# Performance work log

Hardware: AMD Instinct MI355X
Metric: run time of the kernel (lower is better)

Reference implementation:

```python
import jax, jax.numpy as jnp
import numpy as np

N_NODES = 50000
N_EDGES = 800000
EPS = 1e-12


def _l2norm(x):
    # F.normalize(x, p=2, dim=1)
    n = jnp.sqrt(jnp.sum(x * x, axis=1, keepdims=True))
    return x / jnp.maximum(n, EPS)


def _sage_layer(h, src, dst, inv_deg, W_self, W_neigh, b, last):
    # mean aggregation over in-neighbors: gather src feats, scatter-add to dst
    msg = jax.ops.segment_sum(h[src], dst, num_segments=N_NODES)  # [N, d]
    h_neigh = msg * inv_deg  # [N, d]
    rst = h @ W_self + h_neigh @ W_neigh + b
    if not last:
        rst = jax.nn.relu(rst)
        rst = _l2norm(rst)
    return rst


def setup_inputs() -> dict:
    key = jax.random.key(0)
    ks = jax.random.split(key, 10)
    d_in, d_h, d_out = 128, 128, 64
    s = lambda k, sh, fan: jax.random.normal(k, sh, jnp.float32) / np.sqrt(fan)
    return {
        "features": jax.random.normal(ks[0], (N_NODES, d_in), jnp.float32),
        "src": jax.random.randint(ks[1], (N_EDGES,), 0, N_NODES, jnp.int32),
        "dst": jax.random.randint(ks[2], (N_EDGES,), 0, N_NODES, jnp.int32),
        "W_self0": s(ks[3], (d_in, d_h), d_in),
        "W_neigh0": s(ks[4], (d_in, d_h), d_in),
        "b0": jnp.zeros((d_h,), jnp.float32),
        "W_self1": s(ks[5], (d_h, d_h), d_h),
        "W_neigh1": s(ks[6], (d_h, d_h), d_h),
        "b1": jnp.zeros((d_h,), jnp.float32),
        "W_self2": s(ks[7], (d_h, d_out), d_h),
        "W_neigh2": s(ks[8], (d_h, d_out), d_h),
        "b2": jnp.zeros((d_out,), jnp.float32),
    }


def reference(features, src, dst, W_self0, W_neigh0, b0, W_self1, W_neigh1, b1, W_self2, W_neigh2, b2):
    # in-degree for mean aggregation (clamped to avoid div-by-zero)
    deg = jax.ops.segment_sum(jnp.ones((N_EDGES,), jnp.float32), dst, num_segments=N_NODES)
    inv_deg = (1.0 / jnp.maximum(deg, 1.0))[:, None]  # [N,1]
    h = _sage_layer(features, src, dst, inv_deg, W_self0, W_neigh0, b0, last=False)
    h = _sage_layer(h, src, dst, inv_deg, W_self1, W_neigh1, b1, last=False)
    out = _sage_layer(h, src, dst, inv_deg, W_self2, W_neigh2, b2, last=True)
    return out
```

## Files before the change

### kernel.cpp

```cpp
#include <hip/hip_runtime.h>
#include <hip/hip_bf16.h>

#define N_NODES 50000
#define N_EDGES 800000
#define NBUCKET 196
#define NPB 256
#define BUCKET_CAP 7168
#define BUCKET_PAD 8192
#define PART_EDGES 4096
#define PART_BLOCKS ((N_EDGES + PART_EDGES - 1) / PART_EDGES)
#define SENTINEL 0xFFFFFFFFu

typedef __attribute__((ext_vector_type(8))) short bf16x8;
typedef __attribute__((ext_vector_type(4))) float f32x4;

__device__ __forceinline__ float bf2f(unsigned short u) {
    unsigned int x = ((unsigned int)u) << 16;
    return __uint_as_float(x);
}
__device__ __forceinline__ unsigned short f2bf(float f) {
    unsigned int x = __float_as_uint(f);
    unsigned int lsb = (x >> 16) & 1u;
    x += 0x7fffu + lsb;
    return (unsigned short)(x >> 16);
}

#define NF2 ((N_NODES * 64 + 255) / 256)
__global__ __launch_bounds__(256) void k_prep(
        const float* __restrict__ Ws0, const float* __restrict__ Wn0,
        const float* __restrict__ Ws1, const float* __restrict__ Wn1,
        const float* __restrict__ Ws2, const float* __restrict__ Wn2,
        __hip_bfloat16* __restrict__ frag0, __hip_bfloat16* __restrict__ frag1,
        __hip_bfloat16* __restrict__ frag2,
        const float2* __restrict__ fin, unsigned int* __restrict__ fout,
        unsigned int* __restrict__ z1, unsigned int* __restrict__ z2,
        int* __restrict__ cursor, int* __restrict__ valid) {
    int b = blockIdx.x;
    if (b >= 40 + NF2) {
        int tid = threadIdx.x;
        if (tid < NBUCKET) { cursor[tid] = 0; valid[tid] = 0; }
        if (tid < 64)       fout[(size_t)N_NODES * 64 + tid] = 0;
        else if (tid < 128) z1[(size_t)N_NODES * 64 + (tid - 64)] = 0;
        else if (tid < 192) z2[(size_t)N_NODES * 64 + (tid - 128)] = 0;
        return;
    }
    if (b >= 40) {
        int i = (b - 40) * 256 + threadIdx.x;
        if (i < N_NODES * 64) {
            float2 v = fin[i];
            fout[i] = ((unsigned int)f2bf(v.y) << 16) | (unsigned int)f2bf(v.x);
        }
        return;
    }
    const float* Wself;
    const float* Wneigh;
    __hip_bfloat16* frag;
    int Dout, lb;
    if (b < 16)      { Wself = Ws0; Wneigh = Wn0; frag = frag0; Dout = 128; lb = b; }
    else if (b < 32) { Wself = Ws1; Wneigh = Wn1; frag = frag1; Dout = 128; lb = b - 16; }
    else             { Wself = Ws2; Wneigh = Wn2; frag = frag2; Dout = 64;  lb = b - 32; }
    int t = lb * 256 + threadIdx.x;
    int nCt = Dout >> 4;
    int total = nCt * 8 * 64;
    if (t >= total) return;
    int lane = t & 63;
    int kt = (t >> 6) & 7;
    int ct = t >> 9;
    int q = lane >> 4;
    int n = ct * 16 + (lane & 15);
    unsigned short* dstp = (unsigned short*)frag + ((size_t)((ct * 8 + kt) * 64 + lane)) * 8;
    #pragma unroll
    for (int j = 0; j < 8; ++j) {
        int k = kt * 32 + q * 8 + j;
        float v = (k < 128) ? Wself[k * Dout + n] : Wneigh[(k - 128) * Dout + n];
        dstp[j] = f2bf(v);
    }
}

__global__ __launch_bounds__(256) void k_zero(int* __restrict__ cursor, int* __restrict__ valid) {
    int tid = threadIdx.x;
    if (tid < NBUCKET) { cursor[tid] = 0; valid[tid] = 0; }
}

__global__ __launch_bounds__(256) void k_partA(const int* __restrict__ src,
                                               const int* __restrict__ dst,
                                               int* __restrict__ cursor,
                                               int* __restrict__ valid,
                                               unsigned int* __restrict__ bucketArr) {
    __shared__ int hist[NBUCKET];
    __shared__ int base[NBUCKET];
    __shared__ int cnt[NBUCKET];
    int tid = threadIdx.x;
    if (tid < NBUCKET) hist[tid] = 0;
    __syncthreads();
    int e0 = blockIdx.x * PART_EDGES;
    for (int j = 0; j < PART_EDGES; j += 256) {
        int e = e0 + j + tid;
        if (e < N_EDGES) atomicAdd(&hist[dst[e] >> 8], 1);
    }
    __syncthreads();
    if (tid < NBUCKET) {
        int h = hist[tid];
        int hp = (h + 15) & ~15;
        int b0 = atomicAdd(&cursor[tid], hp);
        atomicAdd(&valid[tid], h);
        base[tid] = b0;
        cnt[tid] = 0;
        for (int k = h; k < hp; ++k) {
            int p = b0 + k;
            if (p < BUCKET_CAP) bucketArr[(size_t)tid * BUCKET_CAP + p] = SENTINEL;
        }
    }
    __syncthreads();
    for (int j = 0; j < PART_EDGES; j += 256) {
        int e = e0 + j + tid;
        if (e < N_EDGES) {
            int d = dst[e];
            int b = d >> 8;
            int p = base[b] + atomicAdd(&cnt[b], 1);
            if (p < BUCKET_CAP)
                bucketArr[(size_t)b * BUCKET_CAP + p] =
                    (unsigned int)src[e] | ((unsigned int)(d & 255) << 16);
        }
    }
}

__global__ __launch_bounds__(256) void k_partB(const unsigned int* __restrict__ bucketArr,
                                               const int* __restrict__ cursor,
                                               int* __restrict__ off_beg,
                                               int* __restrict__ off_end,
                                               float* __restrict__ inv_deg,
                                               int* __restrict__ edge_src) {
    __shared__ unsigned int ed[BUCKET_CAP];
    __shared__ int csr[BUCKET_CAP];
    __shared__ int hist[256];
    __shared__ int lbase[256];
    __shared__ int lcnt[256];
    __shared__ int tot_s;
    int b = blockIdx.x;
    int tid = threadIdx.x;
    int size = min(cursor[b], BUCKET_CAP);
    int B0 = b * BUCKET_PAD;
    int nbase = b * NPB;
    int ncount = min(NPB, N_NODES - nbase);
    hist[tid] = 0;
    __syncthreads();
    for (int j = 0; j < BUCKET_CAP; j += 256) {
        int i = j + tid;
        if (i < size) {
            unsigned int u = bucketArr[(size_t)b * BUCKET_CAP + i];
            ed[i] = u;
            if ((u >> 16) < 256u) atomicAdd(&hist[u >> 16], 1);
        }
    }
    __syncthreads();
    int v = hist[tid];
    int pv = (v + 15) & ~15;
    lbase[tid] = pv;
    __syncthreads();
    for (int off = 1; off < 256; off <<= 1) {
        int t = (tid >= off) ? lbase[tid - off] : 0;
        __syncthreads();
        lbase[tid] += t;
        __syncthreads();
    }
    int excl = lbase[tid] - pv;
    if (tid == 255) tot_s = lbase[255];
    __syncthreads();
    lbase[tid] = excl;
    lcnt[tid] = 0;
    if (tid < ncount) {
        off_beg[nbase + tid] = B0 + excl;
        off_end[nbase + tid] = B0 + excl + pv;
        inv_deg[nbase + tid] = 1.0f / (float)max(v, 1);
    }
    __syncthreads();
    int tot = min(tot_s, BUCKET_CAP);
    for (int j = tid; j < tot; j += 256) csr[j] = N_NODES;
    __syncthreads();
    for (int j = 0; j < BUCKET_CAP; j += 256) {
        int i = j + tid;
        if (i < size) {
            unsigned int u = ed[i];
            unsigned int ld = u >> 16;
            if (ld < 256u) {
                int p = lbase[ld] + atomicAdd(&lcnt[ld], 1);
                if (p < BUCKET_CAP) csr[p] = (int)(u & 0xffffu);
            }
        }
    }
    __syncthreads();
    for (int j = tid; j < tot; j += 256) edge_src[B0 + j] = csr[j];
}

__global__ void k_agg(const __hip_bfloat16* __restrict__ hv,
                      const int* __restrict__ off_beg, const int* __restrict__ off_end,
                      const int* __restrict__ edge_src, const float* __restrict__ inv_deg,
                      __hip_bfloat16* __restrict__ msg) {
    int gid = blockIdx.x * blockDim.x + threadIdx.x;
    int node = gid >> 6;
    int lane = gid & 63;
    if (node >= N_NODES) return;
    int quad = lane >> 4;
    int sub = lane & 15;
    int beg = off_beg[node], endp = off_end[node];
    const uint4* hp = (const uint4*)hv;

    float a0[8], a1[8], a2[8], a3[8];
    #pragma unroll
    for (int c = 0; c < 8; ++c) { a0[c] = 0.f; a1[c] = 0.f; a2[c] = 0.f; a3[c] = 0.f; }

    for (int i = beg; i < endp; i += 16) {
        int s0 = edge_src[i + quad];
        int s1 = edge_src[i + 4 + quad];
        int s2 = edge_src[i + 8 + quad];
        int s3 = edge_src[i + 12 + quad];
        uint4 u0 = hp[(size_t)s0 * 16 + sub];
        uint4 u1 = hp[(size_t)s1 * 16 + sub];
        uint4 u2 = hp[(size_t)s2 * 16 + sub];
        uint4 u3 = hp[(size_t)s3 * 16 + sub];
        a0[0] += bf2f((unsigned short)(u0.x & 0xffffu)); a0[1] += bf2f((unsigned short)(u0.x >> 16));
        a0[2] += bf2f((unsigned short)(u0.y & 0xffffu)); a0[3] += bf2f((unsigned short)(u0.y >> 16));
        a0[4] += bf2f((unsigned short)(u0.z & 0xffffu)); a0[5] += bf2f((unsigned short)(u0.z >> 16));
        a0[6] += bf2f((unsigned short)(u0.w & 0xffffu)); a0[7] += bf2f((unsigned short)(u0.w >> 16));
        a1[0] += bf2f((unsigned short)(u1.x & 0xffffu)); a1[1] += bf2f((unsigned short)(u1.x >> 16));
        a1[2] += bf2f((unsigned short)(u1.y & 0xffffu)); a1[3] += bf2f((unsigned short)(u1.y >> 16));
        a1[4] += bf2f((unsigned short)(u1.z & 0xffffu)); a1[5] += bf2f((unsigned short)(u1.z >> 16));
        a1[6] += bf2f((unsigned short)(u1.w & 0xffffu)); a1[7] += bf2f((unsigned short)(u1.w >> 16));
        a2[0] += bf2f((unsigned short)(u2.x & 0xffffu)); a2[1] += bf2f((unsigned short)(u2.x >> 16));
        a2[2] += bf2f((unsigned short)(u2.y & 0xffffu)); a2[3] += bf2f((unsigned short)(u2.y >> 16));
        a2[4] += bf2f((unsigned short)(u2.z & 0xffffu)); a2[5] += bf2f((unsigned short)(u2.z >> 16));
        a2[6] += bf2f((unsigned short)(u2.w & 0xffffu)); a2[7] += bf2f((unsigned short)(u2.w >> 16));
        a3[0] += bf2f((unsigned short)(u3.x & 0xffffu)); a3[1] += bf2f((unsigned short)(u3.x >> 16));
        a3[2] += bf2f((unsigned short)(u3.y & 0xffffu)); a3[3] += bf2f((unsigned short)(u3.y >> 16));
        a3[4] += bf2f((unsigned short)(u3.z & 0xffffu)); a3[5] += bf2f((unsigned short)(u3.z >> 16));
        a3[6] += bf2f((unsigned short)(u3.w & 0xffffu)); a3[7] += bf2f((unsigned short)(u3.w >> 16));
    }

    float r[8];
    #pragma unroll
    for (int c = 0; c < 8; ++c) {
        float t = a0[c] + a1[c] + a2[c] + a3[c];
        t += __shfl_xor(t, 16);
        t += __shfl_xor(t, 32);
        r[c] = t;
    }
    if (quad == 0) {
        float w = inv_deg[node];
        uint4 o;
        o.x = ((unsigned int)f2bf(r[1] * w) << 16) | (unsigned int)f2bf(r[0] * w);
        o.y = ((unsigned int)f2bf(r[3] * w) << 16) | (unsigned int)f2bf(r[2] * w);
        o.z = ((unsigned int)f2bf(r[5] * w) << 16) | (unsigned int)f2bf(r[4] * w);
        o.w = ((unsigned int)f2bf(r[7] * w) << 16) | (unsigned int)f2bf(r[6] * w);
        ((uint4*)msg)[(size_t)node * 16 + sub] = o;
    }
}

template <int NCT, bool LAST>
__global__ __launch_bounds__(256) void k_gemm(const __hip_bfloat16* __restrict__ Aself,
                                              const __hip_bfloat16* __restrict__ Aneigh,
                                              const __hip_bfloat16* __restrict__ frag,
                                              const float* __restrict__ bias,
                                              void* __restrict__ out_) {
    constexpr int Dout = NCT * 16;
    int tid = threadIdx.x;
    int wv = tid >> 6, lane = tid & 63;
    int n0 = blockIdx.x * 64 + wv * 16;
    if (n0 >= N_NODES) return;
    int q = lane >> 4, l15 = lane & 15;
    int rowA = n0 + l15;
    if (rowA > N_NODES - 1) rowA = N_NODES - 1;

    f32x4 acc[NCT];
    #pragma unroll
    for (int c = 0; c < NCT; ++c) acc[c] = (f32x4){0.f, 0.f, 0.f, 0.f};

    const bf16x8* fragv = (const bf16x8*)frag;
    #pragma unroll
    for (int kt = 0; kt < 8; ++kt) {
        int kb = (kt & 3) * 32 + q * 8;
        const __hip_bfloat16* Ab = (kt < 4) ? Aself : Aneigh;
        bf16x8 a = *(const bf16x8*)(Ab + (size_t)rowA * 128 + kb);
        #pragma unroll
        for (int ct = 0; ct < NCT; ++ct) {
            bf16x8 b = fragv[(ct * 8 + kt) * 64 + lane];
            acc[ct] = __builtin_amdgcn_mfma_f32_16x16x32_bf16(a, b, acc[ct], 0, 0, 0);
        }
    }

    float ss[4] = {0.f, 0.f, 0.f, 0.f};
    #pragma unroll
    for (int ct = 0; ct < NCT; ++ct) {
        float bc = bias[ct * 16 + l15];
        #pragma unroll
        for (int r = 0; r < 4; ++r) {
            float v = acc[ct][r] + bc;
            if (!LAST) v = fmaxf(v, 0.0f);
            acc[ct][r] = v;
            ss[r] += v * v;
        }
    }

    float scale[4];
    #pragma unroll
    for (int r = 0; r < 4; ++r) {
        if (!LAST) {
            float s = ss[r];
            s += __shfl_xor(s, 1);
            s += __shfl_xor(s, 2);
            s += __shfl_xor(s, 4);
            s += __shfl_xor(s, 8);
            scale[r] = 1.0f / fmaxf(sqrtf(s), 1e-12f);
        } else {
            scale[r] = 1.0f;
        }
    }

    #pragma unroll
    for (int ct = 0; ct < NCT; ++ct) {
        #pragma unroll
        for (int r = 0; r < 4; ++r) {
            int row = n0 + q * 4 + r;
            if (row < N_NODES) {
                float v = acc[ct][r] * scale[r];
                if (LAST)
                    ((float*)out_)[(size_t)row * Dout + ct * 16 + l15] = v;
                else
                    ((unsigned short*)out_)[(size_t)row * Dout + ct * 16 + l15] = f2bf(v);
            }
        }
    }
}


extern "C" void kernel_launch(void* const* d_in, const int* in_sizes, int n_in,
                              void* d_out, int out_size, void* d_ws, size_t ws_size,
                              hipStream_t stream) {
    const float* features = (const float*)d_in[0];
    const int* src = (const int*)d_in[1];
    const int* dst = (const int*)d_in[2];
    const float* Ws0 = (const float*)d_in[3];
    const float* Wn0 = (const float*)d_in[4];
    const float* b0  = (const float*)d_in[5];
    const float* Ws1 = (const float*)d_in[6];
    const float* Wn1 = (const float*)d_in[7];
    const float* b1  = (const float*)d_in[8];
    const float* Ws2 = (const float*)d_in[9];
    const float* Wn2 = (const float*)d_in[10];
    const float* b2  = (const float*)d_in[11];
    float* out = (float*)d_out;

    char* ws = (char*)d_ws;
    size_t off = 0;
    auto alloc = [&](size_t bytes) -> void* {
        void* p = ws + off;
        off = (off + bytes + 255) & ~(size_t)255;
        return p;
    };
    int*   cursor   = (int*)alloc((size_t)NBUCKET * 4);
    int*   valid    = (int*)alloc((size_t)NBUCKET * 4);
    unsigned int* bucketArr = (unsigned int*)alloc((size_t)NBUCKET * BUCKET_CAP * 4);
    int*   off_beg  = (int*)alloc((size_t)N_NODES * 4);
    int*   off_end  = (int*)alloc((size_t)N_NODES * 4);
    int*   edge_src = (int*)alloc((size_t)NBUCKET * BUCKET_PAD * 4);
    float* inv_deg  = (float*)alloc((size_t)N_NODES * 4);
    __hip_bfloat16* fbf = (__hip_bfloat16*)alloc((size_t)(N_NODES + 1) * 128 * 2);
    __hip_bfloat16* msg = (__hip_bfloat16*)alloc((size_t)N_NODES * 128 * 2);
    __hip_bfloat16* h1  = (__hip_bfloat16*)alloc((size_t)(N_NODES + 1) * 128 * 2);
    __hip_bfloat16* h2  = (__hip_bfloat16*)alloc((size_t)(N_NODES + 1) * 128 * 2);
    __hip_bfloat16* frag0 = (__hip_bfloat16*)alloc((size_t)8 * 8 * 64 * 8 * 2);
    __hip_bfloat16* frag1 = (__hip_bfloat16*)alloc((size_t)8 * 8 * 64 * 8 * 2);
    __hip_bfloat16* frag2 = (__hip_bfloat16*)alloc((size_t)4 * 8 * 64 * 8 * 2);


    k_prep<<<40 + NF2 + 1, 256, 0, stream>>>(Ws0, Wn0, Ws1, Wn1, Ws2, Wn2,
                                             frag0, frag1, frag2,
                                             (const float2*)features, (unsigned int*)fbf,
                                             (unsigned int*)h1, (unsigned int*)h2,
                                             cursor, valid);
    k_partA<<<PART_BLOCKS, 256, 0, stream>>>(src, dst, cursor, valid, bucketArr);
    k_zero<<<1, 256, 0, stream>>>(cursor, valid);
    k_partA<<<PART_BLOCKS, 256, 0, stream>>>(src, dst, cursor, valid, bucketArr);
    k_partB<<<NBUCKET, 256, 0, stream>>>(bucketArr, cursor,
                                         off_beg, off_end, inv_deg, edge_src);

    const int aggGrid = (N_NODES * 64) / 256;
    const int gemmGrid = (N_NODES + 63) / 64;

    k_agg<<<aggGrid, 256, 0, stream>>>(fbf, off_beg, off_end, edge_src, inv_deg, msg);
    k_gemm<8, false><<<gemmGrid, 256, 0, stream>>>(fbf, msg, frag0, b0, h1);
    k_agg<<<aggGrid, 256, 0, stream>>>(h1, off_beg, off_end, edge_src, inv_deg, msg);
    k_gemm<8, false><<<gemmGrid, 256, 0, stream>>>(h1, msg, frag1, b1, h2);
    k_agg<<<aggGrid, 256, 0, stream>>>(h2, off_beg, off_end, edge_src, inv_deg, msg);
    k_gemm<4, true><<<gemmGrid, 256, 0, stream>>>(h2, msg, frag2, b2, out);
}
```

Baseline: 285.8 us.

## Transform-before-aggregate in last layer and drop duplicate partition pass

The last layer now multiplies h2 by W_neigh first, producing 64-wide features, and aggregates those instead of the 128-wide h2. This halves the gather traffic for that layer, at the cost of an extra GEMM kernel and an fp32 intermediate. Separately, the k_partA launch that ran before k_zero is removed along with the k_zero kernel, so partitioning now runs once using the zeroing already done in k_prep. The change also rounds W_neigh·h2 to bf16 before aggregation, which shifts the numerics slightly.

New measurement: 265.8 us. 7.0% less time.

```diff
diff --git a/kernel.cpp b/kernel.cpp
--- a/kernel.cpp
+++ b/kernel.cpp
@@ -34,6 +34,7 @@
         __hip_bfloat16* __restrict__ frag2,
         const float2* __restrict__ fin, unsigned int* __restrict__ fout,
         unsigned int* __restrict__ z1, unsigned int* __restrict__ z2,
+        unsigned int* __restrict__ zt,
         int* __restrict__ cursor, int* __restrict__ valid) {
     int b = blockIdx.x;
     if (b >= 40 + NF2) {
@@ -42,6 +43,7 @@
         if (tid < 64)       fout[(size_t)N_NODES * 64 + tid] = 0;
         else if (tid < 128) z1[(size_t)N_NODES * 64 + (tid - 64)] = 0;
         else if (tid < 192) z2[(size_t)N_NODES * 64 + (tid - 128)] = 0;
+        else if (tid < 224) zt[(size_t)N_NODES * 32 + (tid - 192)] = 0;
         return;
     }
     if (b >= 40) {
@@ -75,11 +77,6 @@
         float v = (k < 128) ? Wself[k * Dout + n] : Wneigh[(k - 128) * Dout + n];
         dstp[j] = f2bf(v);
     }
-}
-
-__global__ __launch_bounds__(256) void k_zero(int* __restrict__ cursor, int* __restrict__ valid) {
-    int tid = threadIdx.x;
-    if (tid < NBUCKET) { cursor[tid] = 0; valid[tid] = 0; }
 }
 
 __global__ __launch_bounds__(256) void k_partA(const int* __restrict__ src,
@@ -256,6 +253,56 @@
     }
 }
 
+__global__ void k_agg64(const __hip_bfloat16* __restrict__ tv,
+                        const int* __restrict__ off_beg, const int* __restrict__ off_end,
+                        const int* __restrict__ edge_src, const float* __restrict__ inv_deg,
+                        float* __restrict__ g) {
+    int gid = blockIdx.x * blockDim.x + threadIdx.x;
+    int node = gid >> 6;
+    int lane = gid & 63;
+    if (node >= N_NODES) return;
+    int oct = lane >> 3;
+    int sub8 = lane & 7;
+    int beg = off_beg[node], endp = off_end[node];
+    const uint4* tp = (const uint4*)tv;
+
+    float a0[8], a1[8];
+    #pragma unroll
+    for (int c = 0; c < 8; ++c) { a0[c] = 0.f; a1[c] = 0.f; }
+
+    for (int i = beg; i < endp; i += 16) {
+        int s0 = edge_src[i + oct];
+        int s1 = edge_src[i + 8 + oct];
+        uint4 u0 = tp[(size_t)s0 * 8 + sub8];
+        uint4 u1 = tp[(size_t)s1 * 8 + sub8];
+        a0[0] += bf2f((unsigned short)(u0.x & 0xffffu)); a0[1] += bf2f((unsigned short)(u0.x >> 16));
+        a0[2] += bf2f((unsigned short)(u0.y & 0xffffu)); a0[3] += bf2f((unsigned short)(u0.y >> 16));
+        a0[4] += bf2f((unsigned short)(u0.z & 0xffffu)); a0[5] += bf2f((unsigned short)(u0.z >> 16));
+        a0[6] += bf2f((unsigned short)(u0.w & 0xffffu)); a0[7] += bf2f((unsigned short)(u0.w >> 16));
+        a1[0] += bf2f((unsigned short)(u1.x & 0xffffu)); a1[1] += bf2f((unsigned short)(u1.x >> 16));
+        a1[2] += bf2f((unsigned short)(u1.y & 0xffffu)); a1[3] += bf2f((unsigned short)(u1.y >> 16));
+        a1[4] += bf2f((unsigned short)(u1.z & 0xffffu)); a1[5] += bf2f((unsigned short)(u1.z >> 16));
+        a1[6] += bf2f((unsigned short)(u1.w & 0xffffu)); a1[7] += bf2f((unsigned short)(u1.w >> 16));
+    }
+
+    float r[8];
+    #pragma unroll
+    for (int c = 0; c < 8; ++c) {
+        float t = a0[c] + a1[c];
+        t += __shfl_xor(t, 8);
+        t += __shfl_xor(t, 16);
+        t += __shfl_xor(t, 32);
+        r[c] = t;
+    }
+    if (oct == 0) {
+        float w = inv_deg[node];
+        float4 o1 = {r[0] * w, r[1] * w, r[2] * w, r[3] * w};
+        float4 o2 = {r[4] * w, r[5] * w, r[6] * w, r[7] * w};
+        ((float4*)g)[(size_t)node * 16 + sub8 * 2]     = o1;
+        ((float4*)g)[(size_t)node * 16 + sub8 * 2 + 1] = o2;
+    }
+}
+
 template <int NCT, bool LAST>
 __global__ __launch_bounds__(256) void k_gemm(const __hip_bfloat16* __restrict__ Aself,
                                               const __hip_bfloat16* __restrict__ Aneigh,
@@ -327,6 +374,85 @@
                     ((float*)out_)[(size_t)row * Dout + ct * 16 + l15] = v;
                 else
                     ((unsigned short*)out_)[(size_t)row * Dout + ct * 16 + l15] = f2bf(v);
+            }
+        }
+    }
+}
+
+__global__ __launch_bounds__(256) void k_gemmT(const __hip_bfloat16* __restrict__ h,
+                                               const __hip_bfloat16* __restrict__ frag,
+                                               __hip_bfloat16* __restrict__ t_out) {
+    int tid = threadIdx.x;
+    int wv = tid >> 6, lane = tid & 63;
+    int n0 = blockIdx.x * 64 + wv * 16;
+    if (n0 >= N_NODES) return;
+    int q = lane >> 4, l15 = lane & 15;
+    int rowA = n0 + l15;
+    if (rowA > N_NODES - 1) rowA = N_NODES - 1;
+
+    f32x4 acc[4];
+    #pragma unroll
+    for (int c = 0; c < 4; ++c) acc[c] = (f32x4){0.f, 0.f, 0.f, 0.f};
+
+    const bf16x8* fragv = (const bf16x8*)frag;
+    #pragma unroll
+    for (int kt = 0; kt < 4; ++kt) {
+        int kb = kt * 32 + q * 8;
+        bf16x8 a = *(const bf16x8*)(h + (size_t)rowA * 128 + kb);
+        #pragma unroll
+        for (int ct = 0; ct < 4; ++ct) {
+            bf16x8 b = fragv[(ct * 8 + kt + 4) * 64 + lane];
+            acc[ct] = __builtin_amdgcn_mfma_f32_16x16x32_bf16(a, b, acc[ct], 0, 0, 0);
+        }
+    }
+    #pragma unroll
+    for (int ct = 0; ct < 4; ++ct) {
+        #pragma unroll
+        for (int r = 0; r < 4; ++r) {
+            int row = n0 + q * 4 + r;
+            if (row < N_NODES)
+                ((unsigned short*)t_out)[(size_t)row * 64 + ct * 16 + l15] = f2bf(acc[ct][r]);
+        }
+    }
+}
+
+__global__ __launch_bounds__(256) void k_gemmS(const __hip_bfloat16* __restrict__ h,
+                                               const __hip_bfloat16* __restrict__ frag,
+                                               const float* __restrict__ bias,
+                                               const float* __restrict__ g,
+                                               float* __restrict__ out) {
+    int tid = threadIdx.x;
+    int wv = tid >> 6, lane = tid & 63;
+    int n0 = blockIdx.x * 64 + wv * 16;
+    if (n0 >= N_NODES) return;
+    int q = lane >> 4, l15 = lane & 15;
+    int rowA = n0 + l15;
+    if (rowA > N_NODES - 1) rowA = N_NODES - 1;
+
+    f32x4 acc[4];
+    #pragma unroll
+    for (int c = 0; c < 4; ++c) acc[c] = (f32x4){0.f, 0.f, 0.f, 0.f};
+
+    const bf16x8* fragv = (const bf16x8*)frag;
+    #pragma unroll
+    for (int kt = 0; kt < 4; ++kt) {
+        int kb = kt * 32 + q * 8;
+        bf16x8 a = *(const bf16x8*)(h + (size_t)rowA * 128 + kb);
+        #pragma unroll
+        for (int ct = 0; ct < 4; ++ct) {
+            bf16x8 b = fragv[(ct * 8 + kt) * 64 + lane];
+            acc[ct] = __builtin_amdgcn_mfma_f32_16x16x32_bf16(a, b, acc[ct], 0, 0, 0);
+        }
+    }
+    #pragma unroll
+    for (int ct = 0; ct < 4; ++ct) {
+        float bc = bias[ct * 16 + l15];
+        #pragma unroll
+        for (int r = 0; r < 4; ++r) {
+            int row = n0 + q * 4 + r;
+            if (row < N_NODES) {
+                float v = acc[ct][r] + bc + g[(size_t)row * 64 + ct * 16 + l15];
+                out[(size_t)row * 64 + ct * 16 + l15] = v;
             }
         }
     }
@@ -368,18 +494,18 @@
     __hip_bfloat16* msg = (__hip_bfloat16*)alloc((size_t)N_NODES * 128 * 2);
     __hip_bfloat16* h1  = (__hip_bfloat16*)alloc((size_t)(N_NODES + 1) * 128 * 2);
     __hip_bfloat16* h2  = (__hip_bfloat16*)alloc((size_t)(N_NODES + 1) * 128 * 2);
+    __hip_bfloat16* t2  = (__hip_bfloat16*)alloc((size_t)(N_NODES + 1) * 64 * 2);
+    float* g   = (float*)alloc((size_t)N_NODES * 64 * 4);
     __hip_bfloat16* frag0 = (__hip_bfloat16*)alloc((size_t)8 * 8 * 64 * 8 * 2);
     __hip_bfloat16* frag1 = (__hip_bfloat16*)alloc((size_t)8 * 8 * 64 * 8 * 2);
     __hip_bfloat16* frag2 = (__hip_bfloat16*)alloc((size_t)4 * 8 * 64 * 8 * 2);
-
 
     k_prep<<<40 + NF2 + 1, 256, 0, stream>>>(Ws0, Wn0, Ws1, Wn1, Ws2, Wn2,
                                              frag0, frag1, frag2,
                                              (const float2*)features, (unsigned int*)fbf,
                                              (unsigned int*)h1, (unsigned int*)h2,
+                                             (unsigned int*)t2,
                                              cursor, valid);
-    k_partA<<<PART_BLOCKS, 256, 0, stream>>>(src, dst, cursor, valid, bucketArr);
-    k_zero<<<1, 256, 0, stream>>>(cursor, valid);
     k_partA<<<PART_BLOCKS, 256, 0, stream>>>(src, dst, cursor, valid, bucketArr);
     k_partB<<<NBUCKET, 256, 0, stream>>>(bucketArr, cursor,
                                          off_beg, off_end, inv_deg, edge_src);
@@ -391,6 +517,7 @@
     k_gemm<8, false><<<gemmGrid, 256, 0, stream>>>(fbf, msg, frag0, b0, h1);
     k_agg<<<aggGrid, 256, 0, stream>>>(h1, off_beg, off_end, edge_src, inv_deg, msg);
     k_gemm<8, false><<<gemmGrid, 256, 0, stream>>>(h1, msg, frag1, b1, h2);
-    k_agg<<<aggGrid, 256, 0, stream>>>(h2, off_beg, off_end, edge_src, inv_deg, msg);
-    k_gemm<4, true><<<gemmGrid, 256, 0, stream>>>(h2, msg, frag2, b2, out);
-}
+    k_gemmT<<<gemmGrid, 256, 0, stream>>>(h2, frag2, t2);
+    k_agg64<<<aggGrid, 256, 0, stream>>>(t2, off_beg, off_end, edge_src, inv_deg, g);
+    k_gemmS<<<gemmGrid, 256, 0, stream>>>(h2, frag2, b2, g, out);
+}
```
